# Kernel optimization log

Measured on AMD Instinct MI355X. Metric: run time of the kernel, lower is better.

Reference implementation:

```python
import jax, jax.numpy as jnp
import numpy as np

B, D, C = 16384, 1024, 2048


def setup_inputs() -> dict:
    key = jax.random.key(0)
    k1, k2 = jax.random.split(key)
    x = jax.random.normal(k1, (B, D), dtype=jnp.float32)
    # xavier_uniform for centers of shape (C, D): bound = sqrt(6/(C+D))
    bound = float(np.sqrt(6.0 / (C + D)))
    centers = jax.random.uniform(k2, (C, D), dtype=jnp.float32, minval=-bound, maxval=bound)
    gamma = jnp.ones((1,), dtype=jnp.float32)
    return {"x": x, "centers": centers, "gamma": gamma}


def _rbf(x, centers, gamma):
    # then Euclidean norm (sqrt) and exp(-gamma * dist) as in the torch module.
    x2 = jnp.sum(x * x, axis=-1, keepdims=True)            # (B, 1)
    c2 = jnp.sum(centers * centers, axis=-1)               # (C,)
    sq = x2 - 2.0 * jnp.einsum('bd,cd->bc', x, centers) + c2[None, :]
    dist = jnp.sqrt(jnp.maximum(sq, 0.0))                  # (B, C)
    return jnp.exp(-gamma[0] * dist)


def reference(x, centers, gamma):
    return _rbf(x, centers, gamma)
```

## Files before the change

kernel.cpp:

```cpp
#include <hip/hip_runtime.h>
#include <stdint.h>


typedef __attribute__((ext_vector_type(4))) int i32x4;

#define BM 256
#define BN 256
#define BK 64

__global__ __launch_bounds__(256) void prep_i8(
    const float* __restrict__ in, unsigned char* __restrict__ qb,
    float2* __restrict__ info, int K) {
  int row = blockIdx.x;
  int tid = threadIdx.x;
  float4 v = ((const float4*)(in + (size_t)row * K))[tid];
  float ss = v.x * v.x + v.y * v.y + v.z * v.z + v.w * v.w;
  float am = fmaxf(fmaxf(fabsf(v.x), fabsf(v.y)), fmaxf(fabsf(v.z), fabsf(v.w)));
  for (int off = 32; off > 0; off >>= 1) {
    ss += __shfl_down(ss, off, 64);
    am = fmaxf(am, __shfl_down(am, off, 64));
  }
  __shared__ float pss[4], pam[4], sbc;
  int lane = tid & 63, w = tid >> 6;
  if (lane == 0) { pss[w] = ss; pam[w] = am; }
  __syncthreads();
  if (tid == 0) {
    float tss = pss[0] + pss[1] + pss[2] + pss[3];
    float tam = fmaxf(fmaxf(pam[0], pam[1]), fmaxf(pam[2], pam[3]));
    float s = tam > 0.f ? 127.f / tam : 0.f;
    info[row] = make_float2(tss, tam * (1.f / 127.f));
    sbc = s;
  }
  __syncthreads();
  float s = sbc;
  int qx = __float2int_rn(v.x * s), qy = __float2int_rn(v.y * s);
  int qz = __float2int_rn(v.z * s), qw = __float2int_rn(v.w * s);
  unsigned u = (unsigned)(qx & 255) | ((unsigned)(qy & 255) << 8) |
               ((unsigned)(qz & 255) << 16) | ((unsigned)(qw & 255) << 24);
  ((unsigned*)qb)[(size_t)row * (K >> 2) + tid] = u;
}

#define GLDS(gptr, lptr)                                                      \
  __builtin_amdgcn_global_load_lds(                                           \
      (const __attribute__((address_space(1))) unsigned int*)(gptr),          \
      (__attribute__((address_space(3))) unsigned int*)(lptr), 16, 0, 0)

#define DSR(dst, addr, imm)                                                   \
  asm volatile("ds_read_b128 %0, %1 offset:%c2"                              \
               : "=v"(dst) : "v"(addr), "i"(imm))

#define BARRIER __builtin_amdgcn_s_barrier()
#define LGKM0                                                                 \
  do {                                                                        \
    asm volatile("s_waitcnt lgkmcnt(0)" ::: "memory");                        \
    __builtin_amdgcn_sched_barrier(0);                                        \
  } while (0)
#define VMW(n) asm volatile("s_waitcnt vmcnt(" #n ")" ::: "memory")

#define MFMAI8(a, b, c) __builtin_amdgcn_mfma_i32_16x16x64_i8((a), (b), (c), 0, 0, 0)

__global__ __launch_bounds__(512, 1) void rbf_gemm_i8(
    const unsigned char* __restrict__ A, const unsigned char* __restrict__ Bm,
    const float2* __restrict__ xinfo, const float2* __restrict__ cinfo,
    const float* __restrict__ gamma, float* __restrict__ out,
    int M, int N, int K) {
  __shared__ __align__(16) unsigned char lds[3 * 32768];

  int nbn = N / BN;
  int nwg = (M / BM) * nbn;
  int bid = blockIdx.x;
  int wg = bid;
  if ((nwg & 7) == 0) {
    int cpx = nwg >> 3;
    wg = (bid & 7) * cpx + (bid >> 3);
  }
  int bm = wg / nbn, bn = wg % nbn;

  int tid = threadIdx.x;
  int lane = tid & 63, wv = tid >> 6;
  int wm = wv >> 2;
  int wn = wv & 3;
  int l15 = lane & 15, l4 = lane >> 4;

  const size_t Kz = (size_t)K;

  int pr = tid >> 2;
  int lr = pr ^ ((pr >> 2) & 1);
  int ls = (tid & 3) ^ (lr & 3);
  const unsigned char* AgT = A + (size_t)bm * BM * Kz + (size_t)lr * Kz + ls * 16;
  const unsigned char* BgT = Bm + (size_t)bn * BN * Kz + (size_t)lr * Kz + ls * 16;
  size_t rstep = (size_t)128 * Kz;

#define STG_A(TAU, BUFS)                                                      \
  do {                                                                        \
    GLDS(AgT + (size_t)(TAU) * 64, (BUFS) + tid * 16);                        \
    GLDS(AgT + rstep + (size_t)(TAU) * 64, (BUFS) + 8192 + tid * 16);         \
  } while (0)
#define STG_B(TAU, BUFS)                                                      \
  do {                                                                        \
    GLDS(BgT + (size_t)(TAU) * 64, (BUFS) + 16384 + tid * 16);                \
    GLDS(BgT + rstep + (size_t)(TAU) * 64, (BUFS) + 24576 + tid * 16);        \
  } while (0)

  int sl15 = l15 ^ ((l15 >> 2) & 1);
  int fsl = l4 ^ (l15 & 3);
  unsigned ldsBase =
      (unsigned)(size_t)(const __attribute__((address_space(3))) void*)&lds[0];
  unsigned aBase = ldsBase + (unsigned)(wm * 8192 + sl15 * 64 + fsl * 16);
  unsigned bBase = ldsBase + (unsigned)(16384 + wn * 4096 + sl15 * 64 + fsl * 16);

  i32x4 acc[8][4];
#pragma unroll
  for (int m = 0; m < 8; ++m)
#pragma unroll
    for (int n = 0; n < 4; ++n) acc[m][n] = (i32x4){0, 0, 0, 0};

  int nt = K / BK;

  STG_A(0, lds); STG_B(0, lds);
  STG_A(1, lds + 32768); STG_B(1, lds + 32768);
  VMW(4);
  BARRIER;

  int rb = 0;
  for (int t = 0; t < nt; ++t) {
    unsigned bufOff = (unsigned)rb * 32768u;
    int sbi = rb + 2; if (sbi >= 3) sbi -= 3;
    unsigned char* bufS = lds + sbi * 32768;
    bool doStage = (t + 2 < nt);

    unsigned aAd = aBase + bufOff;
    unsigned bAd = bBase + bufOff;

    i32x4 a0, a1, a2, a3, b0, b1, b2, b3;
    DSR(a0, aAd, 0);    DSR(a1, aAd, 1024);
    DSR(a2, aAd, 2048); DSR(a3, aAd, 3072);
    DSR(b0, bAd, 0);    DSR(b1, bAd, 1024);
    DSR(b2, bAd, 2048); DSR(b3, bAd, 3072);
    if (doStage) STG_A(t + 2, bufS);
    BARRIER;
    LGKM0;
    __builtin_amdgcn_s_setprio(1);
    acc[0][0] = MFMAI8(a0, b0, acc[0][0]);
    acc[0][1] = MFMAI8(a0, b1, acc[0][1]);
    acc[0][2] = MFMAI8(a0, b2, acc[0][2]);
    acc[0][3] = MFMAI8(a0, b3, acc[0][3]);
    acc[1][0] = MFMAI8(a1, b0, acc[1][0]);
    acc[1][1] = MFMAI8(a1, b1, acc[1][1]);
    acc[1][2] = MFMAI8(a1, b2, acc[1][2]);
    acc[1][3] = MFMAI8(a1, b3, acc[1][3]);
    acc[2][0] = MFMAI8(a2, b0, acc[2][0]);
    acc[2][1] = MFMAI8(a2, b1, acc[2][1]);
    acc[2][2] = MFMAI8(a2, b2, acc[2][2]);
    acc[2][3] = MFMAI8(a2, b3, acc[2][3]);
    acc[3][0] = MFMAI8(a3, b0, acc[3][0]);
    acc[3][1] = MFMAI8(a3, b1, acc[3][1]);
    acc[3][2] = MFMAI8(a3, b2, acc[3][2]);
    acc[3][3] = MFMAI8(a3, b3, acc[3][3]);
    __builtin_amdgcn_s_setprio(0);
    BARRIER;

    i32x4 a4, a5, a6, a7;
    DSR(a4, aAd, 4096); DSR(a5, aAd, 5120);
    DSR(a6, aAd, 6144); DSR(a7, aAd, 7168);
    if (doStage) STG_B(t + 2, bufS);
    BARRIER;
    LGKM0;
    __builtin_amdgcn_s_setprio(1);
    acc[4][0] = MFMAI8(a4, b0, acc[4][0]);
    acc[4][1] = MFMAI8(a4, b1, acc[4][1]);
    acc[4][2] = MFMAI8(a4, b2, acc[4][2]);
    acc[4][3] = MFMAI8(a4, b3, acc[4][3]);
    acc[5][0] = MFMAI8(a5, b0, acc[5][0]);
    acc[5][1] = MFMAI8(a5, b1, acc[5][1]);
    acc[5][2] = MFMAI8(a5, b2, acc[5][2]);
    acc[5][3] = MFMAI8(a5, b3, acc[5][3]);
    acc[6][0] = MFMAI8(a6, b0, acc[6][0]);
    acc[6][1] = MFMAI8(a6, b1, acc[6][1]);
    acc[6][2] = MFMAI8(a6, b2, acc[6][2]);
    acc[6][3] = MFMAI8(a6, b3, acc[6][3]);
    acc[7][0] = MFMAI8(a7, b0, acc[7][0]);
    acc[7][1] = MFMAI8(a7, b1, acc[7][1]);
    acc[7][2] = MFMAI8(a7, b2, acc[7][2]);
    acc[7][3] = MFMAI8(a7, b3, acc[7][3]);
    __builtin_amdgcn_s_setprio(0);
    if (t < nt - 2) {
      VMW(4);
      BARRIER;
    } else if (t == nt - 2) {
      VMW(0);
      BARRIER;
    }

    rb++; if (rb == 3) rb = 0;
  }

  float g = gamma[0];
  int rb0 = bm * BM + wm * 128 + l4 * 4;
  int cb0 = bn * BN + wn * 64 + l15;
#pragma unroll
  for (int m = 0; m < 8; ++m) {
#pragma unroll
    for (int j = 0; j < 4; ++j) {
      int row = rb0 + m * 16 + j;
      float2 xi = xinfo[row];
      size_t ob = (size_t)row * N;
#pragma unroll
      for (int n = 0; n < 4; ++n) {
        int col = cb0 + n * 16;
        float2 ci = cinfo[col];
        float dot = (float)acc[m][n][j] * xi.y * ci.y;
        float sq = fmaxf(xi.x + ci.x - 2.f * dot, 0.f);
        out[ob + col] = __expf(-g * __builtin_sqrtf(sq));
      }
    }
  }
}

__global__ __launch_bounds__(256) void rbf_naive(
    const float* __restrict__ x, const float* __restrict__ cent,
    const float* __restrict__ gamma, float* __restrict__ out, int D, int N) {
  int row = blockIdx.x;
  int col = blockIdx.y * blockDim.x + threadIdx.x;
  extern __shared__ float xs[];
  for (int i = threadIdx.x; i < D; i += blockDim.x)
    xs[i] = x[(size_t)row * D + i];
  __syncthreads();
  if (col >= N) return;
  const float* cp = cent + (size_t)col * D;
  float s = 0.f;
  for (int d = 0; d < D; ++d) {
    float df = xs[d] - cp[d];
    s += df * df;
  }
  out[(size_t)row * N + col] = __expf(-gamma[0] * __builtin_sqrtf(fmaxf(s, 0.f)));
}

extern "C" void kernel_launch(void* const* d_in, const int* in_sizes, int n_in,
                              void* d_out, int out_size, void* d_ws, size_t ws_size,
                              hipStream_t stream) {
  const float* x = (const float*)d_in[0];
  const float* cent = (const float*)d_in[1];
  const float* gamma = (const float*)d_in[2];
  float* out = (float*)d_out;

  const int D = 1024;
  int Brows = in_sizes[0] / D;
  int C = in_sizes[1] / D;

  size_t qa = (size_t)Brows * D;
  size_t qc = (size_t)C * D;
  size_t need = qa + qc + (size_t)Brows * 8 + (size_t)C * 8;
  bool can = (ws_size >= need) && (D == 1024) && (Brows % BM == 0) &&
             (C % BN == 0);

  if (!can) {
    dim3 grid(Brows, (C + 255) / 256);
    hipLaunchKernelGGL(rbf_naive, grid, dim3(256), D * sizeof(float), stream,
                       x, cent, gamma, out, D, C);
    return;
  }

  unsigned char* xb = (unsigned char*)d_ws;
  unsigned char* cb = xb + qa;
  float2* xinfo = (float2*)(xb + qa + qc);
  float2* cinfo = xinfo + Brows;

  hipLaunchKernelGGL(prep_i8, dim3(Brows), dim3(256), 0, stream, x, xb, xinfo, D);
  hipLaunchKernelGGL(prep_i8, dim3(C), dim3(256), 0, stream, cent, cb, cinfo, D);

  int nwg = (Brows / BM) * (C / BN);
  hipLaunchKernelGGL(rbf_gemm_i8, dim3(nwg), dim3(512), 0, stream,
                     xb, cb, xinfo, cinfo, gamma, out, Brows, C, D);
}
```

Before: 91.27 us.

## Shrink int8 GEMM tile to 128x128 with 256-thread blocks

Reduces the workgroup tile from 256x256 to 128x128 with 4 waves instead of 8, each wave owning a 64x64 output block. Staging of A and B is merged into one step per K-tile, and the mid-iteration barriers are removed. The smaller LDS footprint (48KB) and lower register use allow multiple workgroups per CU and give more workgroups for load balance. The cost is lower operand reuse per loaded byte and more global/L2 traffic.

After: 89.67 us. About the same (-1.8%).

```diff
diff --git a/kernel.cpp b/kernel.cpp
--- a/kernel.cpp
+++ b/kernel.cpp
@@ -4,8 +4,8 @@
 
 typedef __attribute__((ext_vector_type(4))) int i32x4;
 
-#define BM 256
-#define BN 256
+#define BM 128
+#define BN 128
 #define BK 64
 
 __global__ __launch_bounds__(256) void prep_i8(
@@ -59,12 +59,12 @@
 
 #define MFMAI8(a, b, c) __builtin_amdgcn_mfma_i32_16x16x64_i8((a), (b), (c), 0, 0, 0)
 
-__global__ __launch_bounds__(512, 1) void rbf_gemm_i8(
+__global__ __launch_bounds__(256) void rbf_gemm_i8(
     const unsigned char* __restrict__ A, const unsigned char* __restrict__ Bm,
     const float2* __restrict__ xinfo, const float2* __restrict__ cinfo,
     const float* __restrict__ gamma, float* __restrict__ out,
     int M, int N, int K) {
-  __shared__ __align__(16) unsigned char lds[3 * 32768];
+  __shared__ __align__(16) unsigned char lds[3 * 16384];
 
   int nbn = N / BN;
   int nwg = (M / BM) * nbn;
@@ -78,8 +78,8 @@
 
   int tid = threadIdx.x;
   int lane = tid & 63, wv = tid >> 6;
-  int wm = wv >> 2;
-  int wn = wv & 3;
+  int wm = wv >> 1;
+  int wn = wv & 1;
   int l15 = lane & 15, l4 = lane >> 4;
 
   const size_t Kz = (size_t)K;
@@ -89,45 +89,41 @@
   int ls = (tid & 3) ^ (lr & 3);
   const unsigned char* AgT = A + (size_t)bm * BM * Kz + (size_t)lr * Kz + ls * 16;
   const unsigned char* BgT = Bm + (size_t)bn * BN * Kz + (size_t)lr * Kz + ls * 16;
-  size_t rstep = (size_t)128 * Kz;
-
-#define STG_A(TAU, BUFS)                                                      \
+  size_t rstep = (size_t)64 * Kz;
+
+#define STG4(TAU, BUFS)                                                       \
   do {                                                                        \
     GLDS(AgT + (size_t)(TAU) * 64, (BUFS) + tid * 16);                        \
-    GLDS(AgT + rstep + (size_t)(TAU) * 64, (BUFS) + 8192 + tid * 16);         \
-  } while (0)
-#define STG_B(TAU, BUFS)                                                      \
-  do {                                                                        \
-    GLDS(BgT + (size_t)(TAU) * 64, (BUFS) + 16384 + tid * 16);                \
-    GLDS(BgT + rstep + (size_t)(TAU) * 64, (BUFS) + 24576 + tid * 16);        \
+    GLDS(AgT + rstep + (size_t)(TAU) * 64, (BUFS) + 4096 + tid * 16);         \
+    GLDS(BgT + (size_t)(TAU) * 64, (BUFS) + 8192 + tid * 16);                 \
+    GLDS(BgT + rstep + (size_t)(TAU) * 64, (BUFS) + 12288 + tid * 16);        \
   } while (0)
 
   int sl15 = l15 ^ ((l15 >> 2) & 1);
   int fsl = l4 ^ (l15 & 3);
   unsigned ldsBase =
       (unsigned)(size_t)(const __attribute__((address_space(3))) void*)&lds[0];
-  unsigned aBase = ldsBase + (unsigned)(wm * 8192 + sl15 * 64 + fsl * 16);
-  unsigned bBase = ldsBase + (unsigned)(16384 + wn * 4096 + sl15 * 64 + fsl * 16);
-
-  i32x4 acc[8][4];
-#pragma unroll
-  for (int m = 0; m < 8; ++m)
+  unsigned aBase = ldsBase + (unsigned)(wm * 4096 + sl15 * 64 + fsl * 16);
+  unsigned bBase = ldsBase + (unsigned)(8192 + wn * 4096 + sl15 * 64 + fsl * 16);
+
+  i32x4 acc[4][4];
+#pragma unroll
+  for (int m = 0; m < 4; ++m)
 #pragma unroll
     for (int n = 0; n < 4; ++n) acc[m][n] = (i32x4){0, 0, 0, 0};
 
   int nt = K / BK;
 
-  STG_A(0, lds); STG_B(0, lds);
-  STG_A(1, lds + 32768); STG_B(1, lds + 32768);
+  STG4(0, lds);
+  STG4(1, lds + 16384);
   VMW(4);
   BARRIER;
 
   int rb = 0;
   for (int t = 0; t < nt; ++t) {
-    unsigned bufOff = (unsigned)rb * 32768u;
+    unsigned bufOff = (unsigned)rb * 16384u;
     int sbi = rb + 2; if (sbi >= 3) sbi -= 3;
-    unsigned char* bufS = lds + sbi * 32768;
-    bool doStage = (t + 2 < nt);
+    unsigned char* bufS = lds + sbi * 16384;
 
     unsigned aAd = aBase + bufOff;
     unsigned bAd = bBase + bufOff;
@@ -137,8 +133,7 @@
     DSR(a2, aAd, 2048); DSR(a3, aAd, 3072);
     DSR(b0, bAd, 0);    DSR(b1, bAd, 1024);
     DSR(b2, bAd, 2048); DSR(b3, bAd, 3072);
-    if (doStage) STG_A(t + 2, bufS);
-    BARRIER;
+    if (t + 2 < nt) STG4(t + 2, bufS);
     LGKM0;
     __builtin_amdgcn_s_setprio(1);
     acc[0][0] = MFMAI8(a0, b0, acc[0][0]);
@@ -158,32 +153,7 @@
     acc[3][2] = MFMAI8(a3, b2, acc[3][2]);
     acc[3][3] = MFMAI8(a3, b3, acc[3][3]);
     __builtin_amdgcn_s_setprio(0);
-    BARRIER;
-
-    i32x4 a4, a5, a6, a7;
-    DSR(a4, aAd, 4096); DSR(a5, aAd, 5120);
-    DSR(a6, aAd, 6144); DSR(a7, aAd, 7168);
-    if (doStage) STG_B(t + 2, bufS);
-    BARRIER;
-    LGKM0;
-    __builtin_amdgcn_s_setprio(1);
-    acc[4][0] = MFMAI8(a4, b0, acc[4][0]);
-    acc[4][1] = MFMAI8(a4, b1, acc[4][1]);
-    acc[4][2] = MFMAI8(a4, b2, acc[4][2]);
-    acc[4][3] = MFMAI8(a4, b3, acc[4][3]);
-    acc[5][0] = MFMAI8(a5, b0, acc[5][0]);
-    acc[5][1] = MFMAI8(a5, b1, acc[5][1]);
-    acc[5][2] = MFMAI8(a5, b2, acc[5][2]);
-    acc[5][3] = MFMAI8(a5, b3, acc[5][3]);
-    acc[6][0] = MFMAI8(a6, b0, acc[6][0]);
-    acc[6][1] = MFMAI8(a6, b1, acc[6][1]);
-    acc[6][2] = MFMAI8(a6, b2, acc[6][2]);
-    acc[6][3] = MFMAI8(a6, b3, acc[6][3]);
-    acc[7][0] = MFMAI8(a7, b0, acc[7][0]);
-    acc[7][1] = MFMAI8(a7, b1, acc[7][1]);
-    acc[7][2] = MFMAI8(a7, b2, acc[7][2]);
-    acc[7][3] = MFMAI8(a7, b3, acc[7][3]);
-    __builtin_amdgcn_s_setprio(0);
+
     if (t < nt - 2) {
       VMW(4);
       BARRIER;
@@ -196,10 +166,10 @@
   }
 
   float g = gamma[0];
-  int rb0 = bm * BM + wm * 128 + l4 * 4;
+  int rb0 = bm * BM + wm * 64 + l4 * 4;
   int cb0 = bn * BN + wn * 64 + l15;
 #pragma unroll
-  for (int m = 0; m < 8; ++m) {
+  for (int m = 0; m < 4; ++m) {
 #pragma unroll
     for (int j = 0; j < 4; ++j) {
       int row = rb0 + m * 16 + j;
@@ -270,6 +240,6 @@
   hipLaunchKernelGGL(prep_i8, dim3(C), dim3(256), 0, stream, cent, cb, cinfo, D);
 
   int nwg = (Brows / BM) * (C / BN);
-  hipLaunchKernelGGL(rbf_gemm_i8, dim3(nwg), dim3(512), 0, stream,
+  hipLaunchKernelGGL(rbf_gemm_i8, dim3(nwg), dim3(256), 0, stream,
                      xb, cb, xinfo, cinfo, gamma, out, Brows, C, D);
 }
```

## Switch int8 GEMM from triple to double LDS buffering with fewer barriers

Applied to the files above, without the earlier changes.

Replaces the three-stage LDS ring with two 32KB buffers and merges the separate A and B staging steps into one prefetch of the next K tile. All A/B fragments are read up front, and a partial lgkmcnt wait lets the first half of the MFMAs start while the remaining reads finish. This leaves one barrier per iteration instead of three. The launch-bounds minimum is dropped and the LDS footprint shrinks, which may allow more co-resident work, but the full vmcnt(0) wait each iteration exposes more global-load latency.

New measurement: 89.10 us. -2.4%, faster.

```diff
diff --git a/kernel.cpp b/kernel.cpp
--- a/kernel.cpp
+++ b/kernel.cpp
@@ -50,21 +50,21 @@
                : "=v"(dst) : "v"(addr), "i"(imm))
 
 #define BARRIER __builtin_amdgcn_s_barrier()
-#define LGKM0                                                                 \
+#define LGKM(n)                                                               \
   do {                                                                        \
-    asm volatile("s_waitcnt lgkmcnt(0)" ::: "memory");                        \
+    asm volatile("s_waitcnt lgkmcnt(" #n ")" ::: "memory");                   \
     __builtin_amdgcn_sched_barrier(0);                                        \
   } while (0)
 #define VMW(n) asm volatile("s_waitcnt vmcnt(" #n ")" ::: "memory")
 
 #define MFMAI8(a, b, c) __builtin_amdgcn_mfma_i32_16x16x64_i8((a), (b), (c), 0, 0, 0)
 
-__global__ __launch_bounds__(512, 1) void rbf_gemm_i8(
+__global__ __launch_bounds__(512) void rbf_gemm_i8(
     const unsigned char* __restrict__ A, const unsigned char* __restrict__ Bm,
     const float2* __restrict__ xinfo, const float2* __restrict__ cinfo,
     const float* __restrict__ gamma, float* __restrict__ out,
     int M, int N, int K) {
-  __shared__ __align__(16) unsigned char lds[3 * 32768];
+  __shared__ __align__(16) unsigned char lds[2 * 32768];
 
   int nbn = N / BN;
   int nwg = (M / BM) * nbn;
@@ -91,13 +91,10 @@
   const unsigned char* BgT = Bm + (size_t)bn * BN * Kz + (size_t)lr * Kz + ls * 16;
   size_t rstep = (size_t)128 * Kz;
 
-#define STG_A(TAU, BUFS)                                                      \
+#define STG4(TAU, BUFS)                                                       \
   do {                                                                        \
     GLDS(AgT + (size_t)(TAU) * 64, (BUFS) + tid * 16);                        \
     GLDS(AgT + rstep + (size_t)(TAU) * 64, (BUFS) + 8192 + tid * 16);         \
-  } while (0)
-#define STG_B(TAU, BUFS)                                                      \
-  do {                                                                        \
     GLDS(BgT + (size_t)(TAU) * 64, (BUFS) + 16384 + tid * 16);                \
     GLDS(BgT + rstep + (size_t)(TAU) * 64, (BUFS) + 24576 + tid * 16);        \
   } while (0)
@@ -117,29 +114,27 @@
 
   int nt = K / BK;
 
-  STG_A(0, lds); STG_B(0, lds);
-  STG_A(1, lds + 32768); STG_B(1, lds + 32768);
-  VMW(4);
+  STG4(0, lds);
+  VMW(0);
   BARRIER;
 
-  int rb = 0;
   for (int t = 0; t < nt; ++t) {
-    unsigned bufOff = (unsigned)rb * 32768u;
-    int sbi = rb + 2; if (sbi >= 3) sbi -= 3;
-    unsigned char* bufS = lds + sbi * 32768;
-    bool doStage = (t + 2 < nt);
+    unsigned bufOff = (unsigned)(t & 1) * 32768u;
+    unsigned char* bufS = lds + ((t + 1) & 1) * 32768;
 
     unsigned aAd = aBase + bufOff;
     unsigned bAd = bBase + bufOff;
 
-    i32x4 a0, a1, a2, a3, b0, b1, b2, b3;
+    i32x4 a0, a1, a2, a3, a4, a5, a6, a7, b0, b1, b2, b3;
     DSR(a0, aAd, 0);    DSR(a1, aAd, 1024);
     DSR(a2, aAd, 2048); DSR(a3, aAd, 3072);
     DSR(b0, bAd, 0);    DSR(b1, bAd, 1024);
     DSR(b2, bAd, 2048); DSR(b3, bAd, 3072);
-    if (doStage) STG_A(t + 2, bufS);
-    BARRIER;
-    LGKM0;
+    DSR(a4, aAd, 4096); DSR(a5, aAd, 5120);
+    DSR(a6, aAd, 6144); DSR(a7, aAd, 7168);
+    if (t + 1 < nt) STG4(t + 1, bufS);
+
+    LGKM(4);
     __builtin_amdgcn_s_setprio(1);
     acc[0][0] = MFMAI8(a0, b0, acc[0][0]);
     acc[0][1] = MFMAI8(a0, b1, acc[0][1]);
@@ -157,16 +152,7 @@
     acc[3][1] = MFMAI8(a3, b1, acc[3][1]);
     acc[3][2] = MFMAI8(a3, b2, acc[3][2]);
     acc[3][3] = MFMAI8(a3, b3, acc[3][3]);
-    __builtin_amdgcn_s_setprio(0);
-    BARRIER;
-
-    i32x4 a4, a5, a6, a7;
-    DSR(a4, aAd, 4096); DSR(a5, aAd, 5120);
-    DSR(a6, aAd, 6144); DSR(a7, aAd, 7168);
-    if (doStage) STG_B(t + 2, bufS);
-    BARRIER;
-    LGKM0;
-    __builtin_amdgcn_s_setprio(1);
+    LGKM(0);
     acc[4][0] = MFMAI8(a4, b0, acc[4][0]);
     acc[4][1] = MFMAI8(a4, b1, acc[4][1]);
     acc[4][2] = MFMAI8(a4, b2, acc[4][2]);
@@ -184,15 +170,11 @@
     acc[7][2] = MFMAI8(a7, b2, acc[7][2]);
     acc[7][3] = MFMAI8(a7, b3, acc[7][3]);
     __builtin_amdgcn_s_setprio(0);
-    if (t < nt - 2) {
-      VMW(4);
-      BARRIER;
-    } else if (t == nt - 2) {
+
+    if (t < nt - 1) {
       VMW(0);
       BARRIER;
     }
-
-    rb++; if (rb == 3) rb = 0;
   }
 
   float g = gamma[0];
```
